# Kernel tuning notes

Hardware: AMD Instinct MI355X
Metric: run time of the kernel (lower is better)

Reference implementation:

```python
import jax, jax.numpy as jnp
import numpy as np

N, D, C = 8192, 128, 64
MARGIN = 0.5


def setup_inputs() -> dict:
    key = jax.random.key(0)
    k1, k2 = jax.random.split(key)
    embedings = jax.random.normal(k1, (N, D), dtype=jnp.float32)
    targets = jax.random.randint(k2, (N,), 0, C, dtype=jnp.int32)
    return {"embedings": embedings, "targets": targets}


def _triplet_terms(x, targets):
    # pairwise squared distances, faithful to pairwise_distances(y=None):
    xn = jnp.sum(x * x, axis=1)                       # [N]
    d = xn[:, None] + xn[None, :] - 2.0 * (x @ x.T)   # [N, N]
    d = jnp.clip(d - jnp.diagonal(d)[None, :], 0.0)

    same = targets[:, None] == targets[None, :]        # [N, N] bool
    diff = ~same
    BIG = jnp.float32(1e30)
    g_pos = jnp.argmax(jnp.where(same, d, -BIG), axis=1)  # farthest same-class (global idx)
    g_neg = jnp.argmin(jnp.where(diff, d, BIG), axis=1)   # closest other-class (global idx)

    # Faithful to source bug: the mined index is the POSITION WITHIN THE
    # SAME/DIFF-CLASS SUBSET (np.argsort on the masked slice), which the
    # original then uses to index the full embedding batch.
    cum_same = jnp.cumsum(same.astype(jnp.int32), axis=1)
    cum_diff = jnp.cumsum(diff.astype(jnp.int32), axis=1)
    p_pos = jnp.take_along_axis(cum_same, g_pos[:, None], axis=1)[:, 0] - 1
    p_neg = jnp.take_along_axis(cum_diff, g_neg[:, None], axis=1)[:, 0] - 1

    anchors = x
    positives = x[p_pos]
    negatives = x[p_neg]

    valid = (jnp.sum(same, axis=1) > 1) & (jnp.sum(diff, axis=1) >= 1)
    vf = valid.astype(x.dtype)                         # [N]
    vcount = jnp.sum(vf)

    ap = jnp.sum((anchors - positives) ** 2, axis=1)
    an = jnp.sum((anchors - negatives) ** 2, axis=1)
    npd = jnp.sum((positives - negatives) ** 2, axis=1)

    tl = jax.nn.relu(ap - an + MARGIN) * vf
    non_zero = jnp.sum((tl > 0).astype(jnp.int32))
    triplet_term = jnp.where(
        non_zero == 0,
        jnp.sum(tl) / vcount,                                   # mean over valid rows
        jnp.sum(tl) / jnp.maximum(non_zero, 1).astype(x.dtype),  # sum(tl / non_zero)
    )

    l1 = lambda v: jnp.sum(jnp.abs(v) * vf[:, None]) / vcount
    sparse_term = (l1(anchors) + l1(positives) + l1(negatives)) / 3.0

    pairwise_term = jax.nn.relu(jnp.sum((ap - an - npd) * vf) / vcount)

    ap_mean = jnp.sum(ap * vf) / vcount
    an_mean = jnp.sum(an * vf) / vcount
    return triplet_term, sparse_term, pairwise_term, vcount, ap_mean, an_mean


def reference(embedings, targets):
    return _triplet_terms(embedings, targets)
```

## Files before the change

kernel.cpp:

```cpp
#include <hip/hip_runtime.h>
#include <float.h>
#include <stdint.h>

#define NROWS 8192
#define DIM 128
#define KAUG 192
#define MARGIN 0.5f
#define NCHUNK (NROWS / 64)
#define SCH 32
#define RLB (NROWS / 8)

typedef __attribute__((ext_vector_type(8))) short short8;
typedef __attribute__((ext_vector_type(4))) float floatx4;

__device__ __forceinline__ void load_lds16(const void* g, void* l) {
    __builtin_amdgcn_global_load_lds(
        (const __attribute__((address_space(1))) unsigned int*)g,
        (__attribute__((address_space(3))) unsigned int*)l, 16, 0, 0);
}

__device__ __forceinline__ unsigned rne_pack(float v0, float v1) {
    unsigned u0 = __float_as_uint(v0), u1 = __float_as_uint(v1);
    unsigned r0 = (u0 + 0x7fffu + ((u0 >> 16) & 1u)) >> 16;
    unsigned r1 = (u1 + 0x7fffu + ((u1 >> 16) & 1u)) & 0xffff0000u;
    return r0 | r1;
}

__global__ __launch_bounds__(256) void prep_kernel(const float* __restrict__ x,
                                                   const int* __restrict__ tgt,
                                                   uint4* __restrict__ fragA,
                                                   uint4* __restrict__ fragB,
                                                   float* __restrict__ xn,
                                                   float* __restrict__ l1n,
                                                   int* __restrict__ pre,
                                                   int* __restrict__ cc) {
    __shared__ int cntS[NCHUNK][64];
    const int b = blockIdx.x;
    if (b < NROWS / 16) {
        float (*sums)[17] = (float (*)[17])cntS;
        float (*suml)[17] = ((float (*)[17])cntS) + 16;
        const int t = threadIdx.x;
        const int s = t >> 6, lane = t & 63;
        const int rloc = lane & 15, q = lane >> 4;
        const int k0 = s * 32 + q * 8;
        const float* xr = x + (size_t)(b * 16 + rloc) * DIM + k0;
        float4 va = *(const float4*)xr, vb = *(const float4*)(xr + 4);
        float vv[8] = {va.x, va.y, va.z, va.w, vb.x, vb.y, vb.z, vb.w};
        unsigned h[4];
        float ss = 0.f, ll = 0.f;
        #pragma unroll
        for (int e = 0; e < 4; ++e) {
            ss += vv[2 * e] * vv[2 * e] + vv[2 * e + 1] * vv[2 * e + 1];
            ll += fabsf(vv[2 * e]) + fabsf(vv[2 * e + 1]);
            h[e] = rne_pack(vv[2 * e], vv[2 * e + 1]);
        }
        uint4 hv = make_uint4(h[0], h[1], h[2], h[3]);
        fragA[(size_t)(b * 6 + s) * 64 + lane] = hv;
        fragB[(size_t)(b * 6 + s) * 64 + lane] = hv;
        {
            const int ab = t >> 6;
            const unsigned bits = (ab < 2) ? 0x4200u : 0xC200u;
            const int ti = tgt[b * 16 + rloc];
            const int cb = (ab & 1) * 32 + q * 8;
            unsigned hh[4];
            #pragma unroll
            for (int e = 0; e < 4; ++e) {
                unsigned lo = (cb + 2 * e == ti) ? bits : 0u;
                unsigned hi = (cb + 2 * e + 1 == ti) ? bits : 0u;
                hh[e] = lo | (hi << 16);
            }
            uint4* dst = (ab < 2) ? fragA : fragB;
            dst[(size_t)(b * 6 + 4 + (ab & 1)) * 64 + lane] =
                make_uint4(hh[0], hh[1], hh[2], hh[3]);
        }
        const int c16 = s * 4 + q;
        sums[rloc][c16] = ss;
        suml[rloc][c16] = ll;
        __syncthreads();
        if (t < 16) {
            float tot = 0.f;
            #pragma unroll
            for (int c2 = 0; c2 < 16; ++c2) tot += sums[t][c2];
            xn[b * 16 + t] = tot;
        } else if (t < 32) {
            const int tt = t - 16;
            float tot = 0.f;
            #pragma unroll
            for (int c2 = 0; c2 < 16; ++c2) tot += suml[tt][c2];
            l1n[b * 16 + tt] = tot;
        }
    } else {
        const int tid = threadIdx.x;
        for (int f = tid; f < NCHUNK * 64; f += 256) ((int*)cntS)[f] = 0;
        __syncthreads();
        for (int j = tid; j < NROWS; j += 256) atomicAdd(&cntS[j >> 6][tgt[j]], 1);
        __syncthreads();
        if (tid < 64) {
            int run = 0;
            for (int k = 0; k < NCHUNK; ++k) {
                pre[k * 64 + tid] = run;
                run += cntS[k][tid];
            }
            cc[tid] = run;
        }
    }
}

__global__ __launch_bounds__(256, 2) void mine_kernel(const uint4* __restrict__ fragA,
                                                      const uint4* __restrict__ fragB,
                                                      const float* __restrict__ xn,
                                                      float4* __restrict__ part) {
    __shared__ __align__(16) uint4 Sb[1536];
    __shared__ float xnS[64];

    const int tid  = threadIdx.x;
    const int lane = tid & 63;
    const int w    = tid >> 6;
    const int m    = lane & 15;
    const int q    = lane >> 4;
    const int ib     = blockIdx.x & 31;
    const int chunk  = blockIdx.x >> 5;
    const int i0     = ib * 256;
    const int jbase0 = chunk * (NROWS / SCH);

    short8 aih[4][6];
    float xni[4];
    #pragma unroll
    for (int t = 0; t < 4; ++t) {
        const int irow = i0 + w * 64 + t * 16 + m;
        xni[t] = xn[irow];
        const int itile = (i0 >> 4) + w * 4 + t;
        #pragma unroll
        for (int s = 0; s < 6; ++s)
            aih[t][s] = *(const short8*)&fragA[(size_t)(itile * 6 + s) * 64 + lane];
    }

    unsigned kmin[4] = {0xFFFFFFFFu, 0xFFFFFFFFu, 0xFFFFFFFFu, 0xFFFFFFFFu};
    unsigned kmax[4] = {0u, 0u, 0u, 0u};
    const unsigned M = 0xFFFFFF80u;

    for (int jt = 0; jt < (NROWS / SCH) / 64; ++jt) {
        const int j0 = jbase0 + jt * 64;
        __syncthreads();
        const char* g = (const char*)fragB + (size_t)(j0 >> 4) * 6144;
        #pragma unroll
        for (int it = 0; it < 6; ++it)
            load_lds16(g + it * 4096 + tid * 16,
                       (char*)Sb + it * 4096 + w * 1024);
        if (tid < 64) xnS[tid] = xn[j0 + tid] + 1024.0f;
        __syncthreads();

        #pragma unroll
        for (int st = 0; st < 4; ++st) {
            floatx4 acc0 = {0.f, 0.f, 0.f, 0.f};
            floatx4 acc1 = {0.f, 0.f, 0.f, 0.f};
            floatx4 acc2 = {0.f, 0.f, 0.f, 0.f};
            floatx4 acc3 = {0.f, 0.f, 0.f, 0.f};
            #pragma unroll
            for (int s = 0; s < 6; ++s) {
                short8 jh = *(const short8*)&Sb[(st * 6 + s) * 64 + lane];
                acc0 = __builtin_amdgcn_mfma_f32_16x16x32_bf16(jh, aih[0][s], acc0, 0, 0, 0);
                acc1 = __builtin_amdgcn_mfma_f32_16x16x32_bf16(jh, aih[1][s], acc1, 0, 0, 0);
                acc2 = __builtin_amdgcn_mfma_f32_16x16x32_bf16(jh, aih[2][s], acc2, 0, 0, 0);
                acc3 = __builtin_amdgcn_mfma_f32_16x16x32_bf16(jh, aih[3][s], acc3, 0, 0, 0);
            }
            float4 xnj4 = *(const float4*)&xnS[st * 16 + q * 4];
            float xnj[4] = {xnj4.x, xnj4.y, xnj4.z, xnj4.w};
            #pragma unroll
            for (int t = 0; t < 4; ++t) {
                floatx4 acc = (t == 0) ? acc0 : (t == 1) ? acc1 : (t == 2) ? acc2 : acc3;
                #pragma unroll
                for (int r = 0; r < 4; ++r) {
                    const unsigned e = (unsigned)(jt * 16 + st * 4 + r);
                    float v = fmaf(-2.0f, acc[r], xnj[r]);
                    unsigned u = __float_as_uint(v);
                    kmin[t] = min(kmin[t], (u & M) | e);
                    kmax[t] = max(kmax[t], (u & M) | (127u - e));
                }
            }
        }
    }

    #pragma unroll
    for (int t = 0; t < 4; ++t) {
        unsigned e1 = kmin[t] & 127u;
        float dmin = xni[t] + (__uint_as_float(kmin[t] & M) - 1024.0f);
        int jmin = jbase0 + (int)((e1 >> 4) * 64 + ((e1 >> 2) & 3) * 16) + q * 4 + (int)(e1 & 3);
        unsigned e2 = 127u - (kmax[t] & 127u);
        float dmax = xni[t] + (__uint_as_float(kmax[t] & M) - 3072.0f);
        int jmax = jbase0 + (int)((e2 >> 4) * 64 + ((e2 >> 2) & 3) * 16) + q * 4 + (int)(e2 & 3);

        #pragma unroll
        for (int off = 16; off <= 32; off <<= 1) {
            float ox = __shfl_xor(dmax, off, 64);
            int   oj = __shfl_xor(jmax, off, 64);
            if (ox > dmax || (ox == dmax && oj < jmax)) { dmax = ox; jmax = oj; }
            float on = __shfl_xor(dmin, off, 64);
            int  onj = __shfl_xor(jmin, off, 64);
            if (on < dmin || (on == dmin && onj < jmin)) { dmin = on; jmin = onj; }
        }
        if (q == 0) {
            const int irow = i0 + w * 64 + t * 16 + m;
            part[(size_t)irow * SCH + chunk] =
                make_float4(dmax, __int_as_float(jmax), dmin, __int_as_float(jmin));
        }
    }
}

__global__ __launch_bounds__(256) void rl_kernel(const float* __restrict__ x,
                                                 const int* __restrict__ tgt,
                                                 const float4* __restrict__ part,
                                                 const int* __restrict__ cc,
                                                 const int* __restrict__ pre,
                                                 const float* __restrict__ l1n,
                                                 float* __restrict__ bp) {
    __shared__ float s_red[4][8];
    const int tid = threadIdx.x, w = tid >> 6, lane = tid & 63;
    const int r0 = blockIdx.x * 8 + w * 2;

    float bx, bn;
    int bxj, bnj;
    {
        float4 v = part[(size_t)(r0 + (lane >> 5)) * SCH + (lane & 31)];
        bx = v.x; bxj = __float_as_int(v.y);
        bn = v.z; bnj = __float_as_int(v.w);
    }
    #pragma unroll
    for (int off = 1; off <= 16; off <<= 1) {
        float ox = __shfl_xor(bx, off, 64);
        int   oj = __shfl_xor(bxj, off, 64);
        if (ox > bx || (ox == bx && oj < bxj)) { bx = ox; bxj = oj; }
        float on = __shfl_xor(bn, off, 64);
        int  onj = __shfl_xor(bnj, off, 64);
        if (on < bn || (on == bn && onj < bnj)) { bn = on; bnj = onj; }
    }
    const int gp0 = __shfl(bxj, 0, 64),  gn0 = __shfl(bnj, 0, 64);
    const int gp1 = __shfl(bxj, 32, 64), gn1 = __shfl(bnj, 32, 64);
    const int ti0 = tgt[r0], ti1 = tgt[r0 + 1];

    const int tA = tgt[(gp0 & ~63) + lane], tB = tgt[(gn0 & ~63) + lane];
    const int tC = tgt[(gp1 & ~63) + lane], tD = tgt[(gn1 & ~63) + lane];
    const int pA = pre[(gp0 >> 6) * 64 + ti0], pB = pre[(gn0 >> 6) * 64 + ti0];
    const int pC = pre[(gp1 >> 6) * 64 + ti1], pD = pre[(gn1 >> 6) * 64 + ti1];
    const int pp0 = pA + __popcll(__ballot(tA == ti0 && lane < (gp0 & 63)));
    const int sb0 = pB + __popcll(__ballot(tB == ti0 && lane < (gn0 & 63)));
    const int pp1 = pC + __popcll(__ballot(tC == ti1 && lane < (gp1 & 63)));
    const int sb1 = pD + __popcll(__ballot(tD == ti1 && lane < (gn1 & 63)));
    const int pn0 = gn0 - sb0, pn1 = gn1 - sb1;

    const float2 a0 = *(const float2*)(x + (size_t)r0 * DIM + lane * 2);
    const float2 p0 = *(const float2*)(x + (size_t)pp0 * DIM + lane * 2);
    const float2 q0 = *(const float2*)(x + (size_t)pn0 * DIM + lane * 2);
    const float2 a1 = *(const float2*)(x + (size_t)(r0 + 1) * DIM + lane * 2);
    const float2 p1 = *(const float2*)(x + (size_t)pp1 * DIM + lane * 2);
    const float2 q1 = *(const float2*)(x + (size_t)pn1 * DIM + lane * 2);

    float v0 = (a0.x - p0.x) * (a0.x - p0.x) + (a0.y - p0.y) * (a0.y - p0.y);
    float v1 = (a0.x - q0.x) * (a0.x - q0.x) + (a0.y - q0.y) * (a0.y - q0.y);
    float v2 = (p0.x - q0.x) * (p0.x - q0.x) + (p0.y - q0.y) * (p0.y - q0.y);
    float v3 = (a1.x - p1.x) * (a1.x - p1.x) + (a1.y - p1.y) * (a1.y - p1.y);
    float v4 = (a1.x - q1.x) * (a1.x - q1.x) + (a1.y - q1.y) * (a1.y - q1.y);
    float v5 = (p1.x - q1.x) * (p1.x - q1.x) + (p1.y - q1.y) * (p1.y - q1.y);
    #pragma unroll
    for (int off = 32; off > 0; off >>= 1) {
        v0 += __shfl_xor(v0, off, 64);
        v1 += __shfl_xor(v1, off, 64);
        v2 += __shfl_xor(v2, off, 64);
        v3 += __shfl_xor(v3, off, 64);
        v4 += __shfl_xor(v4, off, 64);
        v5 += __shfl_xor(v5, off, 64);
    }

    if (lane == 0) {
        const float l10 = l1n[r0] + l1n[pp0] + l1n[pn0];
        const float l11 = l1n[r0 + 1] + l1n[pp1] + l1n[pn1];
        const int c0 = cc[ti0], c1 = cc[ti1];
        const float vf0 = (c0 > 1) ? 1.0f : 0.0f;
        const float vf1 = (c1 > 1) ? 1.0f : 0.0f;
        const float tl0 = fmaxf(v0 - v1 + MARGIN, 0.0f) * vf0;
        const float tl1 = fmaxf(v3 - v4 + MARGIN, 0.0f) * vf1;
        s_red[w][0] = tl0 + tl1;
        s_red[w][1] = ((tl0 > 0.f) ? 1.f : 0.f) + ((tl1 > 0.f) ? 1.f : 0.f);
        s_red[w][2] = vf0 + vf1;
        s_red[w][3] = l10 * vf0 + l11 * vf1;
        s_red[w][4] = (v0 - v1 - v2) * vf0 + (v3 - v4 - v5) * vf1;
        s_red[w][5] = v0 * vf0 + v3 * vf1;
        s_red[w][6] = v1 * vf0 + v4 * vf1;
    }
    __syncthreads();
    if (tid < 8)
        bp[blockIdx.x * 8 + tid] =
            s_red[0][tid] + s_red[1][tid] + s_red[2][tid] + s_red[3][tid];
}

__global__ __launch_bounds__(256) void final_kernel(const float* __restrict__ bp,
                                                    float* __restrict__ out) {
    __shared__ float red[32][8];
    const int tid = threadIdx.x, k = tid & 7;
    float s = 0.0f;
    for (int i = tid >> 3; i < RLB; i += 32) s += bp[i * 8 + k];
    red[tid >> 3][k] = s;
    __syncthreads();
    if (tid == 0) {
        float tot[7];
        #pragma unroll
        for (int kk = 0; kk < 7; ++kk) {
            float t = 0.0f;
            for (int i = 0; i < 32; ++i) t += red[i][kk];
            tot[kk] = t;
        }
        float tl = tot[0], nz = tot[1], vc = tot[2], l1 = tot[3];
        float pw = tot[4], apS = tot[5], anS = tot[6];
        out[0] = (nz == 0.0f) ? (tl / vc) : (tl / fmaxf(nz, 1.0f));
        out[1] = (l1 / vc) * (1.0f / 3.0f);
        out[2] = fmaxf(pw / vc, 0.0f);
        out[3] = vc;
        out[4] = apS / vc;
        out[5] = anS / vc;
    }
}

extern "C" void kernel_launch(void* const* d_in, const int* in_sizes, int n_in,
                              void* d_out, int out_size, void* d_ws, size_t ws_size,
                              hipStream_t stream) {
    const float* x   = (const float*)d_in[0];
    const int*   tgt = (const int*)d_in[1];
    float* out = (float*)d_out;
    char*  ws  = (char*)d_ws;

    const size_t fragBytes = (size_t)NROWS * KAUG * 2;
    size_t off = 0;
    uint4* fragA = (uint4*)ws;                  off += fragBytes;
    uint4* fragB = (uint4*)(ws + off);          off += fragBytes;
    float* xn    = (float*)(ws + off);          off += (size_t)NROWS * 4;
    float* l1n   = (float*)(ws + off);          off += (size_t)NROWS * 4;
    int*   pre   = (int*)(ws + off);            off += (size_t)NCHUNK * 64 * 4;
    int*   cc    = (int*)(ws + off);            off += 64 * 4;
    float* bp    = (float*)(ws + off);          off += (size_t)RLB * 8 * 4;
    float4* part = (float4*)(ws + off);         off += (size_t)NROWS * SCH * 16;

    prep_kernel<<<NROWS / 16 + 1, 256, 0, stream>>>(x, tgt, fragA, fragB,
                                                    xn, l1n, pre, cc);
    mine_kernel<<<32 * SCH, 256, 0, stream>>>(fragA, fragB, xn, part);
    rl_kernel<<<RLB, 256, 0, stream>>>(x, tgt, part, cc, pre, l1n, bp);
    final_kernel<<<1, 256, 0, stream>>>(bp, out);
}
```

Baseline: 113.7 us.

## Load B fragments directly to registers with software prefetch, drop LDS staging

The mining kernel no longer stages the j-side bf16 fragments and norms through shared memory with block-wide barriers. Each wave now reads its fragments straight from global memory into registers and double-buffers the next 16-column tile while the current tile's MFMAs and min/max scan run. Index encoding is simplified to match the new flat 16-iteration loop. This removes the __syncthreads and LDS traffic, but every wave now fetches the same B data separately and more registers are live.

```diff
diff --git a/kernel.cpp b/kernel.cpp
--- a/kernel.cpp
+++ b/kernel.cpp
@@ -12,12 +12,6 @@
 
 typedef __attribute__((ext_vector_type(8))) short short8;
 typedef __attribute__((ext_vector_type(4))) float floatx4;
-
-__device__ __forceinline__ void load_lds16(const void* g, void* l) {
-    __builtin_amdgcn_global_load_lds(
-        (const __attribute__((address_space(1))) unsigned int*)g,
-        (__attribute__((address_space(3))) unsigned int*)l, 16, 0, 0);
-}
 
 __device__ __forceinline__ unsigned rne_pack(float v0, float v1) {
     unsigned u0 = __float_as_uint(v0), u1 = __float_as_uint(v1);
@@ -110,9 +104,6 @@
                                                       const uint4* __restrict__ fragB,
                                                       const float* __restrict__ xn,
                                                       float4* __restrict__ part) {
-    __shared__ __align__(16) uint4 Sb[1536];
-    __shared__ float xnS[64];
-
     const int tid  = threadIdx.x;
     const int lane = tid & 63;
     const int w    = tid >> 6;
@@ -122,6 +113,7 @@
     const int chunk  = blockIdx.x >> 5;
     const int i0     = ib * 256;
     const int jbase0 = chunk * (NROWS / SCH);
+    const int jt16   = jbase0 >> 4;
 
     short8 aih[4][6];
     float xni[4];
@@ -139,56 +131,59 @@
     unsigned kmax[4] = {0u, 0u, 0u, 0u};
     const unsigned M = 0xFFFFFF80u;
 
-    for (int jt = 0; jt < (NROWS / SCH) / 64; ++jt) {
-        const int j0 = jbase0 + jt * 64;
-        __syncthreads();
-        const char* g = (const char*)fragB + (size_t)(j0 >> 4) * 6144;
-        #pragma unroll
-        for (int it = 0; it < 6; ++it)
-            load_lds16(g + it * 4096 + tid * 16,
-                       (char*)Sb + it * 4096 + w * 1024);
-        if (tid < 64) xnS[tid] = xn[j0 + tid] + 1024.0f;
-        __syncthreads();
-
-        #pragma unroll
-        for (int st = 0; st < 4; ++st) {
-            floatx4 acc0 = {0.f, 0.f, 0.f, 0.f};
-            floatx4 acc1 = {0.f, 0.f, 0.f, 0.f};
-            floatx4 acc2 = {0.f, 0.f, 0.f, 0.f};
-            floatx4 acc3 = {0.f, 0.f, 0.f, 0.f};
+    short8 jcur[6];
+    #pragma unroll
+    for (int s = 0; s < 6; ++s)
+        jcur[s] = *(const short8*)&fragB[(size_t)(jt16 * 6 + s) * 64 + lane];
+    float4 xnj4 = *(const float4*)&xn[jbase0 + q * 4];
+
+    #pragma unroll 1
+    for (int u = 0; u < 16; ++u) {
+        const int un = (u < 15) ? u + 1 : u;
+        short8 jnxt[6];
+        #pragma unroll
+        for (int s = 0; s < 6; ++s)
+            jnxt[s] = *(const short8*)&fragB[(size_t)((jt16 + un) * 6 + s) * 64 + lane];
+        float4 xnj4n = *(const float4*)&xn[jbase0 + un * 16 + q * 4];
+
+        floatx4 acc0 = {0.f, 0.f, 0.f, 0.f};
+        floatx4 acc1 = {0.f, 0.f, 0.f, 0.f};
+        floatx4 acc2 = {0.f, 0.f, 0.f, 0.f};
+        floatx4 acc3 = {0.f, 0.f, 0.f, 0.f};
+        #pragma unroll
+        for (int s = 0; s < 6; ++s) {
+            acc0 = __builtin_amdgcn_mfma_f32_16x16x32_bf16(jcur[s], aih[0][s], acc0, 0, 0, 0);
+            acc1 = __builtin_amdgcn_mfma_f32_16x16x32_bf16(jcur[s], aih[1][s], acc1, 0, 0, 0);
+            acc2 = __builtin_amdgcn_mfma_f32_16x16x32_bf16(jcur[s], aih[2][s], acc2, 0, 0, 0);
+            acc3 = __builtin_amdgcn_mfma_f32_16x16x32_bf16(jcur[s], aih[3][s], acc3, 0, 0, 0);
+        }
+        const float xnj[4] = {xnj4.x + 1024.0f, xnj4.y + 1024.0f,
+                              xnj4.z + 1024.0f, xnj4.w + 1024.0f};
+        #pragma unroll
+        for (int t = 0; t < 4; ++t) {
+            floatx4 acc = (t == 0) ? acc0 : (t == 1) ? acc1 : (t == 2) ? acc2 : acc3;
             #pragma unroll
-            for (int s = 0; s < 6; ++s) {
-                short8 jh = *(const short8*)&Sb[(st * 6 + s) * 64 + lane];
-                acc0 = __builtin_amdgcn_mfma_f32_16x16x32_bf16(jh, aih[0][s], acc0, 0, 0, 0);
-                acc1 = __builtin_amdgcn_mfma_f32_16x16x32_bf16(jh, aih[1][s], acc1, 0, 0, 0);
-                acc2 = __builtin_amdgcn_mfma_f32_16x16x32_bf16(jh, aih[2][s], acc2, 0, 0, 0);
-                acc3 = __builtin_amdgcn_mfma_f32_16x16x32_bf16(jh, aih[3][s], acc3, 0, 0, 0);
+            for (int r = 0; r < 4; ++r) {
+                const unsigned e = (unsigned)(u * 4 + r);
+                float v = fmaf(-2.0f, acc[r], xnj[r]);
+                unsigned ub = __float_as_uint(v) & M;
+                kmin[t] = min(kmin[t], ub | e);
+                kmax[t] = max(kmax[t], ub | (127u - e));
             }
-            float4 xnj4 = *(const float4*)&xnS[st * 16 + q * 4];
-            float xnj[4] = {xnj4.x, xnj4.y, xnj4.z, xnj4.w};
-            #pragma unroll
-            for (int t = 0; t < 4; ++t) {
-                floatx4 acc = (t == 0) ? acc0 : (t == 1) ? acc1 : (t == 2) ? acc2 : acc3;
-                #pragma unroll
-                for (int r = 0; r < 4; ++r) {
-                    const unsigned e = (unsigned)(jt * 16 + st * 4 + r);
-                    float v = fmaf(-2.0f, acc[r], xnj[r]);
-                    unsigned u = __float_as_uint(v);
-                    kmin[t] = min(kmin[t], (u & M) | e);
-                    kmax[t] = max(kmax[t], (u & M) | (127u - e));
-                }
-            }
-        }
+        }
+        #pragma unroll
+        for (int s = 0; s < 6; ++s) jcur[s] = jnxt[s];
+        xnj4 = xnj4n;
     }
 
     #pragma unroll
     for (int t = 0; t < 4; ++t) {
         unsigned e1 = kmin[t] & 127u;
         float dmin = xni[t] + (__uint_as_float(kmin[t] & M) - 1024.0f);
-        int jmin = jbase0 + (int)((e1 >> 4) * 64 + ((e1 >> 2) & 3) * 16) + q * 4 + (int)(e1 & 3);
+        int jmin = jbase0 + (int)((e1 >> 2) * 16) + q * 4 + (int)(e1 & 3);
         unsigned e2 = 127u - (kmax[t] & 127u);
         float dmax = xni[t] + (__uint_as_float(kmax[t] & M) - 3072.0f);
-        int jmax = jbase0 + (int)((e2 >> 4) * 64 + ((e2 >> 2) & 3) * 16) + q * 4 + (int)(e2 & 3);
+        int jmax = jbase0 + (int)((e2 >> 2) * 16) + q * 4 + (int)(e2 & 3);
 
         #pragma unroll
         for (int off = 16; off <= 32; off <<= 1) {
```

Measured after the change: 126.5 us. +11.2%, slower.
